# Kernel optimization log

Hardware: AMD Instinct MI355X
Metric: run time of the kernel (lower is better)

The kernel has to match this reference:

```python
import jax, jax.numpy as jnp
import numpy as np

D = 768      # embedding_dim
M = 3072     # mlp_dim
G = 4        # num_expert_groups
E = 8        # experts_per_group
KG = 2       # k_groups
KE = 4       # k_experts
EPS = 1e-6   # gate weight threshold from the torch module


def setup_inputs() -> dict:
    key = jax.random.key(0)
    ks = jax.random.split(key, 9)
    x = jax.random.normal(ks[0], (1, 1024, D), dtype=jnp.float32)
    Wg = jax.random.normal(ks[1], (D, G), dtype=jnp.float32) * 0.02
    bg = jax.random.normal(ks[2], (G,), dtype=jnp.float32) * 0.01
    We = jax.random.normal(ks[3], (G, D, E), dtype=jnp.float32) * 0.02
    be = jax.random.normal(ks[4], (G, E), dtype=jnp.float32) * 0.01
    W1 = jax.random.normal(ks[5], (G, E, D, M), dtype=jnp.float32) * 0.02
    b1 = jax.random.normal(ks[6], (G, E, M), dtype=jnp.float32) * 0.01
    W2 = jax.random.normal(ks[7], (G, E, M, D), dtype=jnp.float32) * 0.02
    b2 = jax.random.normal(ks[8], (G, E, D), dtype=jnp.float32) * 0.01
    return {"x": x, "Wg": Wg, "bg": bg, "We": We, "be": be,
            "W1": W1, "b1": b1, "W2": W2, "b2": b2}


def _topk_gates(logits, k):
    # top-k logits -> softmax over the k entries, then zero out weights < 1e-6
    top, idx = jax.lax.top_k(logits, k)
    gates = jax.nn.softmax(top, axis=-1)
    gates = jnp.where(gates >= EPS, gates, jnp.zeros_like(gates))
    return gates, idx


def reference(x, Wg, bg, We, be, W1, b1, W2, b2):
    orig_shape = x.shape
    xf = x.reshape(-1, D)  # [N, D]

    # ---- level 1: group gating (eval mode: clean logits, no noise) ----
    glog = xf @ Wg + bg                      # [N, G]
    ggates, gidx = _topk_gates(glog, KG)     # [N, KG]
    gw = jnp.einsum('nk,nkg->ng', ggates,
                    jax.nn.one_hot(gidx, G, dtype=xf.dtype))  # dense [N, G]

    # ---- level 2: expert gating within each group ----
    # computed densely for all groups; unselected groups get zero group weight
    elog = jnp.einsum('nd,gde->nge', xf, We) + be  # [N, G, E]
    egates, eidx = _topk_gates(elog, KE)            # [N, G, KE]
    ew = jnp.einsum('ngk,ngke->nge', egates,
                    jax.nn.one_hot(eidx, E, dtype=xf.dtype))  # dense [N, G, E]

    combine = gw[:, :, None] * ew  # [N, G, E] combine weights

    # ---- expert MLPs (dense compute, combine-weighted sum) ----
    y = jnp.zeros_like(xf)
    for g in range(G):  # small fixed loop over expert groups
        h = jax.nn.gelu(jnp.einsum('nd,edm->enm', xf, W1[g]) + b1[g][:, None, :],
                        approximate=False)               # [E, N, M]
        o = jnp.einsum('enm,emd->end', h, W2[g]) + b2[g][:, None, :]  # [E, N, D]
        y = y + jnp.einsum('end,ne->nd', o, combine[:, g, :])
    return y.reshape(orig_shape)
```

## Files before the change

kernel.cpp:

```cpp
#include <hip/hip_runtime.h>
#include <hip/hip_bf16.h>
#include <math.h>

#define NTOK 1024
#define DDIM 768
#define MDIM 3072
#define GN 4
#define EN 8
#define NEXP 32
#define NPAIR 8192
#define EPSW 1e-6f
#define MAXRB 96

typedef __attribute__((ext_vector_type(4))) float f32x4;
typedef __attribute__((ext_vector_type(4))) int   i32x4;
typedef __attribute__((ext_vector_type(4))) unsigned short u16x4;
typedef __attribute__((ext_vector_type(8))) __bf16 bf16x8;

__device__ __forceinline__ unsigned short f2bf(float f) {
  unsigned u = __builtin_bit_cast(unsigned, f);
  u += 0x7FFFu + ((u >> 16) & 1u);
  return (unsigned short)(u >> 16);
}

__device__ __forceinline__ void gld_lds16(const void* g, void* l) {
  __builtin_amdgcn_global_load_lds(
      (const __attribute__((address_space(1))) void*)g,
      (__attribute__((address_space(3))) void*)l, 16, 0, 0);
}

template<int N>
__device__ __forceinline__ void wait_vmcnt() {
  asm volatile("s_waitcnt vmcnt(%0)" :: "n"(N) : "memory");
}

__global__ __launch_bounds__(256) void prep_kernel(
    const float* __restrict__ x, unsigned short* __restrict__ xb,
    float* __restrict__ y, int* __restrict__ ctrl)
{
  const int b = blockIdx.x, tid = threadIdx.x;
  if (b < 192) {
    const int i = (b * 256 + tid) * 16;
#pragma unroll
    for (int j = 0; j < 4; ++j) {
      const f32x4 v = *(const f32x4*)(x + i + j * 4);
      u16x4 p = { f2bf(v.x), f2bf(v.y), f2bf(v.z), f2bf(v.w) };
      *(u16x4*)(xb + i + j * 4) = p;
    }
  } else if (b < 960) {
    ((f32x4*)y)[(b - 192) * 256 + tid] = (f32x4){0.f, 0.f, 0.f, 0.f};
  } else {
    ctrl[tid] = 0;
  }
}

__global__ __launch_bounds__(256) void gating_kernel(
    const float* __restrict__ x, const float* __restrict__ Wg,
    const float* __restrict__ bg, const float* __restrict__ We,
    const float* __restrict__ be, int* __restrict__ counts,
    int* __restrict__ pair_e, float* __restrict__ pair_w)
{
  __shared__ float xr[DDIM];
  __shared__ float logits[36];
  const int n = blockIdx.x;
  const int tid = threadIdx.x;
  const float* xp = x + (size_t)n * DDIM;
  for (int d = tid; d < DDIM; d += 256) xr[d] = xp[d];
  __syncthreads();

  const int w = tid >> 6, lane = tid & 63;
  for (int j = 0; j < 9; ++j) {
    const int o = w + 4 * j;
    float s = 0.f;
    if (o < 4) {
      for (int d = lane; d < DDIM; d += 64) s += xr[d] * Wg[d * GN + o];
    } else {
      const int g = (o - 4) >> 3, e = (o - 4) & 7;
      const float* wp = We + (size_t)g * DDIM * EN + e;
      for (int d = lane; d < DDIM; d += 64) s += xr[d] * wp[d * EN];
    }
    for (int off = 32; off; off >>= 1) s += __shfl_xor(s, off);
    if (lane == 0) logits[o] = s + ((o < 4) ? bg[o] : be[o - 4]);
  }
  __syncthreads();

  if (tid == 0) {
    float gl[4];
    for (int i = 0; i < 4; ++i) gl[i] = logits[i];
    int i0 = 0;
    for (int i = 1; i < 4; ++i) if (gl[i] > gl[i0]) i0 = i;
    int i1 = -1;
    for (int i = 0; i < 4; ++i) {
      if (i == i0) continue;
      if (i1 < 0 || gl[i] > gl[i1]) i1 = i;
    }
    const float m = gl[i0];
    const float e1 = expf(gl[i1] - m);
    const float s2 = 1.f + e1;
    float gv[2] = { 1.f / s2, e1 / s2 };
    int gi[2] = { i0, i1 };
    for (int r = 0; r < 2; ++r) if (gv[r] < EPSW) gv[r] = 0.f;

    for (int r = 0; r < 2; ++r) {
      const int g = gi[r];
      float el[8];
      for (int e = 0; e < 8; ++e) el[e] = logits[4 + g * 8 + e];
      int sel[4];
      for (int q = 0; q < 4; ++q) {
        int best = -1;
        for (int e = 0; e < 8; ++e) {
          bool used = false;
          for (int p = 0; p < q; ++p) if (sel[p] == e) used = true;
          if (used) continue;
          if (best < 0 || el[e] > el[best]) best = e;
        }
        sel[q] = best;
      }
      const float mm = el[sel[0]];
      float ex[4]; float ss = 0.f;
      for (int q = 0; q < 4; ++q) { ex[q] = expf(el[sel[q]] - mm); ss += ex[q]; }
      for (int q = 0; q < 4; ++q) {
        float ew = ex[q] / ss;
        if (ew < EPSW) ew = 0.f;
        const int gbl = g * 8 + sel[q];
        const int j = r * 4 + q;
        pair_e[n * 8 + j] = gbl;
        pair_w[n * 8 + j] = gv[r] * ew;
        atomicAdd(&counts[gbl], 1);
      }
    }
  }
}

__global__ void scan_kernel(const int* __restrict__ counts, int* __restrict__ offsets,
                            int* __restrict__ rb_ge, int* __restrict__ rb_by,
                            int* __restrict__ nrb)
{
  if (threadIdx.x == 0) {
    int a = 0, n = 0;
    for (int e = 0; e < NEXP; ++e) {
      offsets[e] = a;
      const int c = counts[e];
      a += c;
      for (int b = 0; b * 128 < c; ++b) { rb_ge[n] = e; rb_by[n] = b; ++n; }
    }
    *nrb = n;
  }
}

__global__ __launch_bounds__(256) void scatter_kernel(
    const int* __restrict__ pair_e, const float* __restrict__ pair_w,
    const int* __restrict__ offsets, int* __restrict__ cursor,
    int* __restrict__ slot_tok, float* __restrict__ slot_w)
{
  const int idx = blockIdx.x * 256 + threadIdx.x;
  if (idx < NPAIR) {
    const int e = pair_e[idx];
    const int s = offsets[e] + atomicAdd(&cursor[e], 1);
    slot_tok[s] = idx >> 3;
    slot_w[s] = pair_w[idx];
  }
}

template<int R, int C>
__global__ __launch_bounds__(256) void repack_kernel(
    const float* __restrict__ W, unsigned short* __restrict__ Wt)
{
  __shared__ float tile[32][33];
  const int ge = blockIdx.z;
  const int rt = blockIdx.y, ct = blockIdx.x;
  const int tid = threadIdx.x;
  {
    const int r = tid >> 3, c4 = tid & 7;
    const f32x4 v = *(const f32x4*)(W + (size_t)ge * R * C
                                      + (size_t)(rt * 32 + r) * C + ct * 32 + c4 * 4);
#pragma unroll
    for (int j = 0; j < 4; ++j) tile[r][c4 * 4 + j] = v[j];
  }
  __syncthreads();
  {
    const int n = tid >> 3, k4 = tid & 7;
    u16x4 p;
    p.x = f2bf(tile[k4 * 4 + 0][n]);
    p.y = f2bf(tile[k4 * 4 + 1][n]);
    p.z = f2bf(tile[k4 * 4 + 2][n]);
    p.w = f2bf(tile[k4 * 4 + 3][n]);
    *(u16x4*)(Wt + (size_t)ge * R * C + (size_t)(ct * 32 + n) * R + rt * 32 + k4 * 4) = p;
  }
}

template<int K, int NLD, int EPI, int GATHER, int KS>
__global__ __launch_bounds__(256, 4) void moe_gemm_bt2(
    const unsigned short* __restrict__ A, const unsigned short* __restrict__ Bt,
    const float* __restrict__ bias, const int* __restrict__ counts,
    const int* __restrict__ offsets, const float* __restrict__ slot_w,
    const int* __restrict__ slot_tok, const int* __restrict__ rb_ge,
    const int* __restrict__ rb_by, const int* __restrict__ nrb,
    unsigned short* __restrict__ Hout, float* __restrict__ Yout)
{
  constexpr int KC = K / KS;
  constexpr int NT = KC / 32;
  constexpr int ABY = 8192;
  constexpr int BUFB = 16384;

  const int rb = blockIdx.x;
  if (rb >= *nrb) return;
  const int ge = rb_ge[rb];
  const int by = rb_by[rb];
  const int cnt = counts[ge];
  const int off = offsets[ge];
  const int nb = blockIdx.y;
  const int ks = (KS > 1) ? blockIdx.z : 0;
  const int kbase = ks * KC;
  const int tid = threadIdx.x;

  __shared__ __align__(16) unsigned char lds[2 * BUFB];

  const unsigned short* asrc[2];
  const unsigned short* bsrc[2];
#pragma unroll
  for (int i = 0; i < 2; ++i) {
    const int q = tid + 256 * i;
    const int m = q >> 2, c = q & 3;
    const int sc = c ^ ((m ^ (m >> 2)) & 3);
    int gr = by * 128 + m; if (gr >= cnt) gr = cnt - 1;
    const int row = GATHER ? slot_tok[off + gr] : (off + gr);
    asrc[i] = A + (size_t)row * K + kbase + sc * 8;
    bsrc[i] = Bt + (size_t)ge * NLD * K + (size_t)(nb * 128 + m) * K + kbase + sc * 8;
  }

  const int w = tid >> 6, lane = tid & 63;
  const int wr = (w >> 1) * 64, wc = (w & 1) * 64;
  const int l15 = lane & 15, l4 = lane >> 4;
  int aoff[4], boff[4];
#pragma unroll
  for (int mf = 0; mf < 4; ++mf) {
    const int m = wr + mf * 16 + l15;
    aoff[mf] = m * 64 + ((l4 ^ ((m ^ (m >> 2)) & 3)) * 16);
  }
#pragma unroll
  for (int nf = 0; nf < 4; ++nf) {
    const int n = wc + nf * 16 + l15;
    boff[nf] = ABY + n * 64 + ((l4 ^ ((n ^ (n >> 2)) & 3)) * 16);
  }

  f32x4 acc[4][4];
#pragma unroll
  for (int mf = 0; mf < 4; ++mf)
#pragma unroll
    for (int nf = 0; nf < 4; ++nf)
      acc[mf][nf] = (f32x4){0.f, 0.f, 0.f, 0.f};

#define ISSUE(T, B) { _Pragma("unroll") \
    for (int i = 0; i < 2; ++i) { \
      gld_lds16(asrc[i] + (size_t)(T) * 32, lds + (B) * BUFB + (tid + 256 * i) * 16); \
      gld_lds16(bsrc[i] + (size_t)(T) * 32, lds + (B) * BUFB + ABY + (tid + 256 * i) * 16); } }
#define COMPUTE(BASE) { bf16x8 afr[4], bfr[4]; _Pragma("unroll") \
    for (int mf = 0; mf < 4; ++mf) \
      afr[mf] = __builtin_bit_cast(bf16x8, *(const i32x4*)((BASE) + aoff[mf])); \
    _Pragma("unroll") \
    for (int nf = 0; nf < 4; ++nf) \
      bfr[nf] = __builtin_bit_cast(bf16x8, *(const i32x4*)((BASE) + boff[nf])); \
    _Pragma("unroll") \
    for (int mf = 0; mf < 4; ++mf) { _Pragma("unroll") \
      for (int nf = 0; nf < 4; ++nf) \
        acc[mf][nf] = __builtin_amdgcn_mfma_f32_16x16x32_bf16( \
            afr[mf], bfr[nf], acc[mf][nf], 0, 0, 0); } }

  ISSUE(0, 0);
  ISSUE(1, 1);

  for (int t = 0; t < NT; ++t) {
    if (t + 1 < NT) wait_vmcnt<4>(); else wait_vmcnt<0>();
    __builtin_amdgcn_s_barrier();
    asm volatile("" ::: "memory");
    COMPUTE(lds + (t & 1) * BUFB);
    asm volatile("" ::: "memory");
    __builtin_amdgcn_s_barrier();
    if (t + 2 < NT) ISSUE(t + 2, t & 1);
  }
#undef ISSUE
#undef COMPUTE

#pragma unroll
  for (int mf = 0; mf < 4; ++mf) {
    const int rb2 = by * 128 + wr + mf * 16 + l4 * 4;
    if constexpr (EPI == 0) {
#pragma unroll
      for (int nf = 0; nf < 4; ++nf) {
        const int col = nb * 128 + wc + nf * 16 + l15;
        const float bv = bias[(size_t)ge * NLD + col];
#pragma unroll
        for (int j = 0; j < 4; ++j) {
          const int r = rb2 + j;
          if (r < cnt) {
            const float v = acc[mf][nf][j] + bv;
            const float gl = 0.5f * v * (1.f + erff(v * 0.70710678118654752f));
            Hout[(size_t)(off + r) * NLD + col] = f2bf(gl);
          }
        }
      }
    } else {
#pragma unroll
      for (int j = 0; j < 4; ++j) {
        const int r = rb2 + j;
        if (r < cnt) {
          const int slot = off + r;
          const float sw = slot_w[slot];
          const int tok = slot_tok[slot];
#pragma unroll
          for (int nf = 0; nf < 4; ++nf) {
            const int col = nb * 128 + wc + nf * 16 + l15;
            const float bv = (ks == 0) ? bias[(size_t)ge * NLD + col] : 0.f;
            atomicAdd(&Yout[(size_t)tok * DDIM + col], sw * (acc[mf][nf][j] + bv));
          }
        }
      }
    }
  }
}

extern "C" void kernel_launch(void* const* d_in, const int* in_sizes, int n_in,
                              void* d_out, int out_size, void* d_ws, size_t ws_size,
                              hipStream_t stream)
{
  const float* x  = (const float*)d_in[0];
  const float* Wg = (const float*)d_in[1];
  const float* bg = (const float*)d_in[2];
  const float* We = (const float*)d_in[3];
  const float* be = (const float*)d_in[4];
  const float* W1 = (const float*)d_in[5];
  const float* b1 = (const float*)d_in[6];
  const float* W2 = (const float*)d_in[7];
  const float* b2 = (const float*)d_in[8];
  float* y = (float*)d_out;

  char* ws = (char*)d_ws;
  int*   counts   = (int*)(ws + 0);
  int*   offsets  = (int*)(ws + 128);
  int*   cursor   = (int*)(ws + 256);
  int*   nrb      = (int*)(ws + 384);
  int*   rb_ge    = (int*)(ws + 512);
  int*   rb_by    = (int*)(ws + 896);
  int*   pair_e   = (int*)(ws + 2048);
  float* pair_w   = (float*)(ws + 34816);
  int*   slot_tok = (int*)(ws + 67584);
  float* slot_w   = (float*)(ws + 100352);
  unsigned short* xb = (unsigned short*)(ws + 135168);
  unsigned short* H  = (unsigned short*)(ws + 12715008);
  unsigned short* Wt = (unsigned short*)(ws + 63046656);

  prep_kernel<<<961, 256, 0, stream>>>(x, xb, y, (int*)ws);
  gating_kernel<<<NTOK, 256, 0, stream>>>(x, Wg, bg, We, be, counts, pair_e, pair_w);
  scan_kernel<<<1, 64, 0, stream>>>(counts, offsets, rb_ge, rb_by, nrb);
  scatter_kernel<<<NPAIR / 256, 256, 0, stream>>>(pair_e, pair_w, offsets, cursor,
                                                  slot_tok, slot_w);

  repack_kernel<DDIM, MDIM><<<dim3(MDIM / 32, DDIM / 32, NEXP), 256, 0, stream>>>(W1, Wt);
  moe_gemm_bt2<DDIM, MDIM, 0, 1, 1><<<dim3(MAXRB, MDIM / 128, 1), 256, 0, stream>>>(
      xb, Wt, b1, counts, offsets, nullptr, slot_tok, rb_ge, rb_by, nrb, H, nullptr);
  repack_kernel<MDIM, DDIM><<<dim3(DDIM / 32, MDIM / 32, NEXP), 256, 0, stream>>>(W2, Wt);
  moe_gemm_bt2<MDIM, DDIM, 1, 0, 2><<<dim3(MAXRB, DDIM / 128, 2), 256, 0, stream>>>(
      H, Wt, b2, counts, offsets, slot_w, slot_tok, rb_ge, rb_by, nrb, nullptr, y);
}
```

Measured before the change: 551.9 us.

## Fuse prep, gating and both weight repacks into one phase kernel

Merges the bf16 conversion of x, output zeroing, gating and both W1/W2 transpose-repacks into a single large launch with block-index dispatch. W2 now gets its own workspace buffer, so it can be repacked alongside W1 instead of after fc1. This removes several kernel launches and the serialisation between the repacks and the GEMMs. The cost is a larger workspace and branch dispatch inside one very big grid.

Result: faster. 534.3 us (-3.2%).

```diff
diff --git a/kernel.cpp b/kernel.cpp
--- a/kernel.cpp
+++ b/kernel.cpp
@@ -34,11 +34,44 @@
   asm volatile("s_waitcnt vmcnt(%0)" :: "n"(N) : "memory");
 }
 
-__global__ __launch_bounds__(256) void prep_kernel(
+template<int R, int C>
+__device__ __forceinline__ void repack_body(
+    float* tile, const float* __restrict__ W, unsigned short* __restrict__ Wt,
+    int ge, int rt, int ct)
+{
+  const int tid = threadIdx.x;
+  {
+    const int r = tid >> 3, c4 = tid & 7;
+    const f32x4 v = *(const f32x4*)(W + (size_t)ge * R * C
+                                      + (size_t)(rt * 32 + r) * C + ct * 32 + c4 * 4);
+#pragma unroll
+    for (int j = 0; j < 4; ++j) tile[r * 33 + c4 * 4 + j] = v[j];
+  }
+  __syncthreads();
+  {
+    const int n = tid >> 3, k4 = tid & 7;
+    u16x4 p;
+    p.x = f2bf(tile[(k4 * 4 + 0) * 33 + n]);
+    p.y = f2bf(tile[(k4 * 4 + 1) * 33 + n]);
+    p.z = f2bf(tile[(k4 * 4 + 2) * 33 + n]);
+    p.w = f2bf(tile[(k4 * 4 + 3) * 33 + n]);
+    *(u16x4*)(Wt + (size_t)ge * R * C + (size_t)(ct * 32 + n) * R + rt * 32 + k4 * 4) = p;
+  }
+}
+
+__global__ __launch_bounds__(256) void phase1_kernel(
     const float* __restrict__ x, unsigned short* __restrict__ xb,
-    float* __restrict__ y, int* __restrict__ ctrl)
-{
-  const int b = blockIdx.x, tid = threadIdx.x;
+    float* __restrict__ y, int* __restrict__ ctrl,
+    const float* __restrict__ Wg, const float* __restrict__ bg,
+    const float* __restrict__ We, const float* __restrict__ be,
+    int* __restrict__ counts, int* __restrict__ pair_e, float* __restrict__ pair_w,
+    const float* __restrict__ W1, unsigned short* __restrict__ W1t,
+    const float* __restrict__ W2, unsigned short* __restrict__ W2t)
+{
+  __shared__ __align__(16) float shm[1056];
+  const int b = blockIdx.x;
+  const int tid = threadIdx.x;
+
   if (b < 192) {
     const int i = (b * 256 + tid) * 16;
 #pragma unroll
@@ -47,88 +80,96 @@
       u16x4 p = { f2bf(v.x), f2bf(v.y), f2bf(v.z), f2bf(v.w) };
       *(u16x4*)(xb + i + j * 4) = p;
     }
-  } else if (b < 960) {
+    return;
+  }
+  if (b < 960) {
     ((f32x4*)y)[(b - 192) * 256 + tid] = (f32x4){0.f, 0.f, 0.f, 0.f};
-  } else {
+    return;
+  }
+  if (b == 960) {
     ctrl[tid] = 0;
-  }
-}
-
-__global__ __launch_bounds__(256) void gating_kernel(
-    const float* __restrict__ x, const float* __restrict__ Wg,
-    const float* __restrict__ bg, const float* __restrict__ We,
-    const float* __restrict__ be, int* __restrict__ counts,
-    int* __restrict__ pair_e, float* __restrict__ pair_w)
-{
-  __shared__ float xr[DDIM];
-  __shared__ float logits[36];
-  const int n = blockIdx.x;
-  const int tid = threadIdx.x;
-  const float* xp = x + (size_t)n * DDIM;
-  for (int d = tid; d < DDIM; d += 256) xr[d] = xp[d];
-  __syncthreads();
-
-  const int w = tid >> 6, lane = tid & 63;
-  for (int j = 0; j < 9; ++j) {
-    const int o = w + 4 * j;
-    float s = 0.f;
-    if (o < 4) {
-      for (int d = lane; d < DDIM; d += 64) s += xr[d] * Wg[d * GN + o];
-    } else {
-      const int g = (o - 4) >> 3, e = (o - 4) & 7;
-      const float* wp = We + (size_t)g * DDIM * EN + e;
-      for (int d = lane; d < DDIM; d += 64) s += xr[d] * wp[d * EN];
+    return;
+  }
+  if (b < 1985) {
+    float* xr = shm;
+    float* logits = shm + 768;
+    const int n = b - 961;
+    const float* xp = x + (size_t)n * DDIM;
+    for (int d = tid; d < DDIM; d += 256) xr[d] = xp[d];
+    __syncthreads();
+
+    const int w = tid >> 6, lane = tid & 63;
+    for (int j = 0; j < 9; ++j) {
+      const int o = w + 4 * j;
+      float s = 0.f;
+      if (o < 4) {
+        for (int d = lane; d < DDIM; d += 64) s += xr[d] * Wg[d * GN + o];
+      } else {
+        const int g = (o - 4) >> 3, e = (o - 4) & 7;
+        const float* wp = We + (size_t)g * DDIM * EN + e;
+        for (int d = lane; d < DDIM; d += 64) s += xr[d] * wp[d * EN];
+      }
+      for (int off = 32; off; off >>= 1) s += __shfl_xor(s, off);
+      if (lane == 0) logits[o] = s + ((o < 4) ? bg[o] : be[o - 4]);
     }
-    for (int off = 32; off; off >>= 1) s += __shfl_xor(s, off);
-    if (lane == 0) logits[o] = s + ((o < 4) ? bg[o] : be[o - 4]);
-  }
-  __syncthreads();
-
-  if (tid == 0) {
-    float gl[4];
-    for (int i = 0; i < 4; ++i) gl[i] = logits[i];
-    int i0 = 0;
-    for (int i = 1; i < 4; ++i) if (gl[i] > gl[i0]) i0 = i;
-    int i1 = -1;
-    for (int i = 0; i < 4; ++i) {
-      if (i == i0) continue;
-      if (i1 < 0 || gl[i] > gl[i1]) i1 = i;
-    }
-    const float m = gl[i0];
-    const float e1 = expf(gl[i1] - m);
-    const float s2 = 1.f + e1;
-    float gv[2] = { 1.f / s2, e1 / s2 };
-    int gi[2] = { i0, i1 };
-    for (int r = 0; r < 2; ++r) if (gv[r] < EPSW) gv[r] = 0.f;
-
-    for (int r = 0; r < 2; ++r) {
-      const int g = gi[r];
-      float el[8];
-      for (int e = 0; e < 8; ++e) el[e] = logits[4 + g * 8 + e];
-      int sel[4];
-      for (int q = 0; q < 4; ++q) {
-        int best = -1;
-        for (int e = 0; e < 8; ++e) {
-          bool used = false;
-          for (int p = 0; p < q; ++p) if (sel[p] == e) used = true;
-          if (used) continue;
-          if (best < 0 || el[e] > el[best]) best = e;
+    __syncthreads();
+
+    if (tid == 0) {
+      float gl[4];
+      for (int i = 0; i < 4; ++i) gl[i] = logits[i];
+      int i0 = 0;
+      for (int i = 1; i < 4; ++i) if (gl[i] > gl[i0]) i0 = i;
+      int i1 = -1;
+      for (int i = 0; i < 4; ++i) {
+        if (i == i0) continue;
+        if (i1 < 0 || gl[i] > gl[i1]) i1 = i;
+      }
+      const float m = gl[i0];
+      const float e1 = expf(gl[i1] - m);
+      const float s2 = 1.f + e1;
+      float gv[2] = { 1.f / s2, e1 / s2 };
+      int gi[2] = { i0, i1 };
+      for (int r = 0; r < 2; ++r) if (gv[r] < EPSW) gv[r] = 0.f;
+
+      for (int r = 0; r < 2; ++r) {
+        const int g = gi[r];
+        float el[8];
+        for (int e = 0; e < 8; ++e) el[e] = logits[4 + g * 8 + e];
+        int sel[4];
+        for (int q = 0; q < 4; ++q) {
+          int best = -1;
+          for (int e = 0; e < 8; ++e) {
+            bool used = false;
+            for (int p = 0; p < q; ++p) if (sel[p] == e) used = true;
+            if (used) continue;
+            if (best < 0 || el[e] > el[best]) best = e;
+          }
+          sel[q] = best;
         }
-        sel[q] = best;
-      }
-      const float mm = el[sel[0]];
-      float ex[4]; float ss = 0.f;
-      for (int q = 0; q < 4; ++q) { ex[q] = expf(el[sel[q]] - mm); ss += ex[q]; }
-      for (int q = 0; q < 4; ++q) {
-        float ew = ex[q] / ss;
-        if (ew < EPSW) ew = 0.f;
-        const int gbl = g * 8 + sel[q];
-        const int j = r * 4 + q;
-        pair_e[n * 8 + j] = gbl;
-        pair_w[n * 8 + j] = gv[r] * ew;
-        atomicAdd(&counts[gbl], 1);
+        const float mm = el[sel[0]];
+        float ex[4]; float ss = 0.f;
+        for (int q = 0; q < 4; ++q) { ex[q] = expf(el[sel[q]] - mm); ss += ex[q]; }
+        for (int q = 0; q < 4; ++q) {
+          float ew = ex[q] / ss;
+          if (ew < EPSW) ew = 0.f;
+          const int gbl = g * 8 + sel[q];
+          const int j = r * 4 + q;
+          pair_e[n * 8 + j] = gbl;
+          pair_w[n * 8 + j] = gv[r] * ew;
+          atomicAdd(&counts[gbl], 1);
+        }
       }
     }
+    return;
+  }
+  if (b < 75713) {
+    const int i = b - 1985;
+    repack_body<DDIM, MDIM>(shm, W1, W1t, i / 2304, (i / 96) % 24, i % 96);
+    return;
+  }
+  {
+    const int i = b - 75713;
+    repack_body<MDIM, DDIM>(shm, W2, W2t, i / 2304, (i / 24) % 96, i % 24);
   }
 }
 
@@ -162,59 +203,29 @@
   }
 }
 
-template<int R, int C>
-__global__ __launch_bounds__(256) void repack_kernel(
-    const float* __restrict__ W, unsigned short* __restrict__ Wt)
-{
-  __shared__ float tile[32][33];
-  const int ge = blockIdx.z;
-  const int rt = blockIdx.y, ct = blockIdx.x;
-  const int tid = threadIdx.x;
-  {
-    const int r = tid >> 3, c4 = tid & 7;
-    const f32x4 v = *(const f32x4*)(W + (size_t)ge * R * C
-                                      + (size_t)(rt * 32 + r) * C + ct * 32 + c4 * 4);
-#pragma unroll
-    for (int j = 0; j < 4; ++j) tile[r][c4 * 4 + j] = v[j];
-  }
-  __syncthreads();
-  {
-    const int n = tid >> 3, k4 = tid & 7;
-    u16x4 p;
-    p.x = f2bf(tile[k4 * 4 + 0][n]);
-    p.y = f2bf(tile[k4 * 4 + 1][n]);
-    p.z = f2bf(tile[k4 * 4 + 2][n]);
-    p.w = f2bf(tile[k4 * 4 + 3][n]);
-    *(u16x4*)(Wt + (size_t)ge * R * C + (size_t)(ct * 32 + n) * R + rt * 32 + k4 * 4) = p;
-  }
-}
-
 template<int K, int NLD, int EPI, int GATHER, int KS>
-__global__ __launch_bounds__(256, 4) void moe_gemm_bt2(
+__device__ __forceinline__ void gemm_body(
+    unsigned char* lds,
     const unsigned short* __restrict__ A, const unsigned short* __restrict__ Bt,
     const float* __restrict__ bias, const int* __restrict__ counts,
     const int* __restrict__ offsets, const float* __restrict__ slot_w,
     const int* __restrict__ slot_tok, const int* __restrict__ rb_ge,
     const int* __restrict__ rb_by, const int* __restrict__ nrb,
-    unsigned short* __restrict__ Hout, float* __restrict__ Yout)
+    unsigned short* __restrict__ Hout, float* __restrict__ Yout,
+    int rb, int nb, int ks)
 {
   constexpr int KC = K / KS;
   constexpr int NT = KC / 32;
   constexpr int ABY = 8192;
   constexpr int BUFB = 16384;
 
-  const int rb = blockIdx.x;
   if (rb >= *nrb) return;
   const int ge = rb_ge[rb];
   const int by = rb_by[rb];
   const int cnt = counts[ge];
   const int off = offsets[ge];
-  const int nb = blockIdx.y;
-  const int ks = (KS > 1) ? blockIdx.z : 0;
   const int kbase = ks * KC;
   const int tid = threadIdx.x;
-
-  __shared__ __align__(16) unsigned char lds[2 * BUFB];
 
   const unsigned short* asrc[2];
   const unsigned short* bsrc[2];
@@ -320,6 +331,33 @@
   }
 }
 
+__global__ __launch_bounds__(256, 4) void fc1_kernel(
+    const unsigned short* __restrict__ xb, const unsigned short* __restrict__ W1t,
+    const float* __restrict__ b1, const int* __restrict__ counts,
+    const int* __restrict__ offsets, const int* __restrict__ slot_tok,
+    const int* __restrict__ rb_ge, const int* __restrict__ rb_by,
+    const int* __restrict__ nrb, unsigned short* __restrict__ H)
+{
+  __shared__ __align__(16) unsigned char lds[2 * 16384];
+  gemm_body<DDIM, MDIM, 0, 1, 1>(lds, xb, W1t, b1, counts, offsets, nullptr,
+                                 slot_tok, rb_ge, rb_by, nrb, H, nullptr,
+                                 blockIdx.x, blockIdx.y, 0);
+}
+
+__global__ __launch_bounds__(256, 4) void fc2_kernel(
+    const unsigned short* __restrict__ H, const unsigned short* __restrict__ W2t,
+    const float* __restrict__ b2, const int* __restrict__ counts,
+    const int* __restrict__ offsets, const float* __restrict__ slot_w,
+    const int* __restrict__ slot_tok, const int* __restrict__ rb_ge,
+    const int* __restrict__ rb_by, const int* __restrict__ nrb,
+    float* __restrict__ y)
+{
+  __shared__ __align__(16) unsigned char lds[2 * 16384];
+  gemm_body<MDIM, DDIM, 1, 0, 2>(lds, H, W2t, b2, counts, offsets, slot_w,
+                                 slot_tok, rb_ge, rb_by, nrb, nullptr, y,
+                                 blockIdx.x, blockIdx.y, blockIdx.z);
+}
+
 extern "C" void kernel_launch(void* const* d_in, const int* in_sizes, int n_in,
                               void* d_out, int out_size, void* d_ws, size_t ws_size,
                               hipStream_t stream)
@@ -346,20 +384,19 @@
   float* pair_w   = (float*)(ws + 34816);
   int*   slot_tok = (int*)(ws + 67584);
   float* slot_w   = (float*)(ws + 100352);
-  unsigned short* xb = (unsigned short*)(ws + 135168);
-  unsigned short* H  = (unsigned short*)(ws + 12715008);
-  unsigned short* Wt = (unsigned short*)(ws + 63046656);
-
-  prep_kernel<<<961, 256, 0, stream>>>(x, xb, y, (int*)ws);
-  gating_kernel<<<NTOK, 256, 0, stream>>>(x, Wg, bg, We, be, counts, pair_e, pair_w);
+  unsigned short* xb  = (unsigned short*)(ws + 135168);
+  unsigned short* H   = (unsigned short*)(ws + 12715008);
+  unsigned short* W1t = (unsigned short*)(ws + 63046656);
+  unsigned short* W2t = (unsigned short*)(ws + 214041600);
+
+  phase1_kernel<<<961 + 1024 + 2 * 73728, 256, 0, stream>>>(
+      x, xb, y, (int*)ws, Wg, bg, We, be, counts, pair_e, pair_w,
+      W1, W1t, W2, W2t);
   scan_kernel<<<1, 64, 0, stream>>>(counts, offsets, rb_ge, rb_by, nrb);
   scatter_kernel<<<NPAIR / 256, 256, 0, stream>>>(pair_e, pair_w, offsets, cursor,
                                                   slot_tok, slot_w);
-
-  repack_kernel<DDIM, MDIM><<<dim3(MDIM / 32, DDIM / 32, NEXP), 256, 0, stream>>>(W1, Wt);
-  moe_gemm_bt2<DDIM, MDIM, 0, 1, 1><<<dim3(MAXRB, MDIM / 128, 1), 256, 0, stream>>>(
-      xb, Wt, b1, counts, offsets, nullptr, slot_tok, rb_ge, rb_by, nrb, H, nullptr);
-  repack_kernel<MDIM, DDIM><<<dim3(DDIM / 32, MDIM / 32, NEXP), 256, 0, stream>>>(W2, Wt);
-  moe_gemm_bt2<MDIM, DDIM, 1, 0, 2><<<dim3(MAXRB, DDIM / 128, 2), 256, 0, stream>>>(
-      H, Wt, b2, counts, offsets, slot_w, slot_tok, rb_ge, rb_by, nrb, nullptr, y);
-}
+  fc1_kernel<<<dim3(MAXRB, MDIM / 128), 256, 0, stream>>>(
+      xb, W1t, b1, counts, offsets, slot_tok, rb_ge, rb_by, nrb, H);
+  fc2_kernel<<<dim3(MAXRB, DDIM / 128, 2), 256, 0, stream>>>(
+      H, W2t, b2, counts, offsets, slot_w, slot_tok, rb_ge, rb_by, nrb, y);
+}
```
